# Kernel optimization log

Measured on AMD Instinct MI355X. Metric: run time of the kernel, lower is better.

## Reference

```python
import jax, jax.numpy as jnp
import numpy as np

N_NODES = 50000
N_EDGES = 1_600_000
D_IN, D_HID, D_OUT, K = 128, 50, 10, 5


def setup_inputs() -> dict:
    key = jax.random.key(0)
    ks = jax.random.split(key, 6)
    x = jax.random.normal(ks[0], (N_NODES, D_IN), dtype=jnp.float32)
    edge_index = jax.random.randint(ks[1], (2, N_EDGES), 0, N_NODES, dtype=jnp.int64)
    cheb_w = jax.random.normal(ks[2], (K, D_IN, D_HID), dtype=jnp.float32) * 0.05
    cheb_b = jax.random.normal(ks[3], (D_HID,), dtype=jnp.float32) * 0.05
    fc_w = jax.random.normal(ks[4], (D_HID, D_OUT), dtype=jnp.float32) * 0.1
    fc_b = jax.random.normal(ks[5], (D_OUT,), dtype=jnp.float32) * 0.1
    return {"x": x, "edge_index": edge_index, "cheb_w": cheb_w,
            "cheb_b": cheb_b, "fc_w": fc_w, "fc_b": fc_b}


def reference(x, edge_index, cheb_w, cheb_b, fc_w, fc_b):
    # ChebConv (PyG, normalization='sym', lambda_max=2.0):
    # L_hat = 2L/lambda_max - I = -D^{-1/2} A D^{-1/2} (zero diagonal)
    row, col = edge_index[0], edge_index[1]
    n = x.shape[0]
    deg = jax.ops.segment_sum(jnp.ones_like(row, dtype=x.dtype), row, num_segments=n)
    dinv = jnp.where(deg > 0, jax.lax.rsqrt(jnp.maximum(deg, 1.0)), 0.0)
    w = -dinv[row] * dinv[col]  # [E] edge weights of L_hat

    def prop(h):  # L_hat @ h via gather-scale-scatter
        return jax.ops.segment_sum(w[:, None] * h[col], row, num_segments=n)

    tx0 = x
    tx1 = prop(x)
    out = jnp.einsum('ni,io->no', tx0, cheb_w[0]) + jnp.einsum('ni,io->no', tx1, cheb_w[1])
    for k in range(2, K):
        tx2 = 2.0 * prop(tx1) - tx0
        out = out + jnp.einsum('ni,io->no', tx2, cheb_w[k])
        tx0, tx1 = tx1, tx2
    out = out + cheb_b

    h = jax.nn.relu(out)
    logits = h @ fc_w + fc_b
    return jax.nn.log_softmax(logits, axis=1)
```

## Files before the change

kernel.cpp:

```cpp
#include <hip/hip_runtime.h>
#include <hip/hip_fp16.h>

#define N_NODES 50000
#define N_EDGES 1600000
#define D_IN    128
#define D_HID   50
#define D_OUT   10
#define K_CHEB  5

#define P1_BLOCKS 256
#define EPB       (N_EDGES / P1_BLOCKS)
#define NBUCK2    256
#define NB_USED2  196
#define BCAP2     96

#define WH_ELEMS  (K_CHEB * 64 * D_IN)
#define WH_BLOCKS ((WH_ELEMS + 255) / 256)

#define VROW      64
#define VSTRIDE   ((size_t)(N_NODES + 1) * VROW)

typedef _Float16 half8_t __attribute__((ext_vector_type(8)));
typedef float    f32x4_t __attribute__((ext_vector_type(4)));


__global__ __launch_bounds__(256) void pass1_kernel(const int* __restrict__ row,
                                                    const int* __restrict__ col,
                                                    unsigned int* __restrict__ store,
                                                    int* __restrict__ bcnt,
                                                    const float* __restrict__ W,
                                                    __half* __restrict__ Wh,
                                                    __half* __restrict__ v,
                                                    __half* __restrict__ b1) {
    int tid = threadIdx.x;
    int blk = blockIdx.x;
    if (blk >= P1_BLOCKS) {
        int wb = blk - P1_BLOCKS;
        if (wb < WH_BLOCKS) {
            int idx = wb * 256 + tid;
            if (idx < WH_ELEMS) {
                int i = idx & 127;
                int n = (idx >> 7) & 63;
                int t = idx >> 13;
                float vv = (n < D_HID) ? W[t * D_IN * D_HID + i * D_HID + n] : 0.f;
                Wh[idx] = __float2half(vv);
            }
        } else {
            if (tid < VROW) {
                v[4 * VSTRIDE + (size_t)N_NODES * VROW + tid] = __float2half(0.f);
                b1[(size_t)N_NODES * VROW + tid] = __float2half(0.f);
            }
        }
        return;
    }
    __shared__ int cnt[NBUCK2];
    cnt[tid] = 0;
    __syncthreads();
    int base = blk * EPB;
    size_t sb = (size_t)blk * (NBUCK2 * BCAP2);
    for (int i = tid; i < EPB; i += 256) {
        int r = row[base + i];
        int c = col[base + i];
        int b = r >> 8;
        int pos = atomicAdd(&cnt[b], 1);
        if (pos >= BCAP2) pos = BCAP2 - 1;
        store[sb + b * BCAP2 + pos] = ((unsigned int)(r & 255) << 16) | (unsigned int)c;
    }
    __syncthreads();
    bcnt[blk * NBUCK2 + tid] = cnt[tid];
}

__global__ __launch_bounds__(512) void pass2_kernel(const unsigned int* __restrict__ store,
                                                    const int* __restrict__ bcnt,
                                                    int* __restrict__ row_start,
                                                    float* __restrict__ dinv,
                                                    float* __restrict__ dinv2,
                                                    float* __restrict__ sdeg,
                                                    int* __restrict__ ewc) {
    __shared__ int hist[256];
    __shared__ int off[256];
    __shared__ int fill[256];
    __shared__ int sb_part[512];
    __shared__ int pscan[256];
    __shared__ int s_bbase;
    int tid = threadIdx.x;
    int b = blockIdx.x;

    {
        int bt = tid & 255, seg = tid >> 8;
        int sum = 0;
        for (int s = seg * 128; s < seg * 128 + 128; ++s) sum += bcnt[s * NBUCK2 + bt];
        sb_part[tid] = sum;
    }
    __syncthreads();
    if (tid < 256) pscan[tid] = sb_part[tid] + sb_part[256 + tid];
    __syncthreads();
    for (int o = 1; o < 256; o <<= 1) {
        int vv = (tid < 256 && tid >= o) ? pscan[tid - o] : 0;
        __syncthreads();
        if (tid < 256) pscan[tid] += vv;
        __syncthreads();
    }
    if (tid == 0) {
        s_bbase = (b == 0) ? 0 : pscan[b - 1];
        if (b == 0) row_start[N_NODES] = pscan[255];
    }
    if (tid < 256) hist[tid] = 0;
    __syncthreads();
    int bbase_b = s_bbase;

    int strip = tid >> 1;
    int sub   = tid & 1;
    int sn = bcnt[strip * NBUCK2 + b];
    size_t sb = (size_t)strip * (NBUCK2 * BCAP2) + b * BCAP2;
    for (int i = sub; i < sn; i += 2)
        atomicAdd(&hist[store[sb + i] >> 16], 1);
    __syncthreads();
    int d = (tid < 256) ? hist[tid] : 0;
    if (tid < 256) off[tid] = d;
    __syncthreads();
    for (int o = 1; o < 256; o <<= 1) {
        int vv = (tid < 256 && tid >= o) ? off[tid - o] : 0;
        __syncthreads();
        if (tid < 256) off[tid] += vv;
        __syncthreads();
    }
    if (tid < 256) {
        int excl = off[tid] - d + bbase_b;
        hist[tid] = excl;
        fill[tid] = 0;
        int r = (b << 8) + tid;
        if (r < N_NODES) {
            row_start[r] = excl;
            float fd = (float)d;
            dinv[r]  = d ? rsqrtf(fd)  : 0.f;
            dinv2[r] = d ? (1.f / fd)  : 0.f;
            sdeg[r]  = d ? sqrtf(fd)   : 0.f;
        }
    }
    __syncthreads();
    for (int i = sub; i < sn; i += 2) {
        unsigned int vv = store[sb + i];
        int rl = vv >> 16;
        int c = vv & 0xffff;
        int p = atomicAdd(&fill[rl], 1);
        ewc[hist[rl] + p] = c;
    }
}

__global__ __launch_bounds__(256) void vgemm_kernel(const float* __restrict__ x,
                                                    const float* __restrict__ dinv,
                                                    const __half* __restrict__ Wh,
                                                    __half* __restrict__ v) {
    int tid = threadIdx.x;
    int lane = tid & 63;
    int wv = __builtin_amdgcn_readfirstlane(tid >> 6);
    int w = blockIdx.x * 4 + wv;
    int grp = w / 5;
    int t = w - grp * 5;
    int m = lane & 15;
    int quad = lane >> 4;

    int node = grp * 16 + m;
    bool ok = (node < N_NODES);
    int ln = ok ? node : (N_NODES - 1);
    float dv = ok ? dinv[node] : 0.f;

    half8_t bfr[4];
    #pragma unroll
    for (int ks = 0; ks < 4; ++ks) {
        const float4* xr = (const float4*)(x + (size_t)ln * D_IN + ks * 32 + quad * 8);
        float4 fA = xr[0], fB = xr[1];
        half8_t h;
        h[0] = (_Float16)fA.x; h[1] = (_Float16)fA.y;
        h[2] = (_Float16)fA.z; h[3] = (_Float16)fA.w;
        h[4] = (_Float16)fB.x; h[5] = (_Float16)fB.y;
        h[6] = (_Float16)fB.z; h[7] = (_Float16)fB.w;
        bfr[ks] = h;
    }

    const __half* Wt = Wh + t * (64 * D_IN);
    half8_t afr[4][4];
    #pragma unroll
    for (int ks = 0; ks < 4; ++ks) {
        int ko = ks * 32 + quad * 8;
        #pragma unroll
        for (int jt = 0; jt < 4; ++jt)
            afr[ks][jt] = *(const half8_t*)(Wt + (jt * 16 + m) * D_IN + ko);
    }

    f32x4_t acc[4];
    #pragma unroll
    for (int jt = 0; jt < 4; ++jt) acc[jt] = (f32x4_t)0.f;
    #pragma unroll
    for (int ks = 0; ks < 4; ++ks)
        #pragma unroll
        for (int jt = 0; jt < 4; ++jt)
            acc[jt] = __builtin_amdgcn_mfma_f32_16x16x32_f16(afr[ks][jt], bfr[ks], acc[jt], 0, 0, 0);

    if (ok) {
        __half* dst = v + t * VSTRIDE + (size_t)node * VROW + quad * 4;
        #pragma unroll
        for (int jt = 0; jt < 4; ++jt) {
            __half2 h0 = __float22half2_rn(make_float2(acc[jt][0] * dv, acc[jt][1] * dv));
            __half2 h1 = __float22half2_rn(make_float2(acc[jt][2] * dv, acc[jt][3] * dv));
            uint2 u;
            u.x = *(unsigned int*)&h0;
            u.y = *(unsigned int*)&h1;
            *(uint2*)(dst + jt * 16) = u;
        }
    }
}

__global__ __launch_bounds__(512) void prop_kernel(const int* __restrict__ row_start,
                                                   const int* __restrict__ ewc,
                                                   const float* __restrict__ dinv2,
                                                   const __half* __restrict__ src,
                                                   const __half* __restrict__ addv,
                                                   const __half* __restrict__ subv,
                                                   float alphaM, int do_sub,
                                                   __half* __restrict__ dst) {
    int tid = threadIdx.x;
    int lane = tid & 63;
    int wv = __builtin_amdgcn_readfirstlane(tid >> 6);
    int r = blockIdx.x * 8 + wv;
    int e0 = row_start[r], e1 = row_start[r + 1];
    float fac = -alphaM * dinv2[r];
    int l = lane & 7;
    int g = lane >> 3;
    const uint4* src16 = (const uint4*)src;
    float ac[8];
    #pragma unroll
    for (int j = 0; j < 8; ++j) ac[j] = 0.f;
    for (int e = e0; e < e1; e += 32) {
        #pragma unroll
        for (int i = 0; i < 4; ++i) {
            int base = e + 8 * i;
            int c0 = ewc[base + 0];
            int c1 = ewc[base + 1];
            int c2 = ewc[base + 2];
            int c3 = ewc[base + 3];
            int c4 = ewc[base + 4];
            int c5 = ewc[base + 5];
            int c6 = ewc[base + 6];
            int c7 = ewc[base + 7];
            int cA = (g & 1) ? c1 : c0;
            int cB = (g & 1) ? c3 : c2;
            int cC = (g & 1) ? c5 : c4;
            int cD = (g & 1) ? c7 : c6;
            int cE = (g & 2) ? cB : cA;
            int cF = (g & 2) ? cD : cC;
            int cl = (g & 4) ? cF : cE;
            if (base + g >= e1) cl = N_NODES;
            uint4 u = src16[(size_t)cl * 8 + l];
            float2 f0 = __half22float2(*(__half2*)&u.x);
            float2 f1 = __half22float2(*(__half2*)&u.y);
            float2 f2 = __half22float2(*(__half2*)&u.z);
            float2 f3 = __half22float2(*(__half2*)&u.w);
            ac[0] += f0.x; ac[1] += f0.y; ac[2] += f1.x; ac[3] += f1.y;
            ac[4] += f2.x; ac[5] += f2.y; ac[6] += f3.x; ac[7] += f3.y;
        }
    }
    #pragma unroll
    for (int k = 8; k <= 32; k <<= 1) {
        #pragma unroll
        for (int j = 0; j < 8; ++j) ac[j] += __shfl_xor(ac[j], k);
    }
    if (g == 0) {
        size_t o = (size_t)r * 8 + l;
        uint4 av = ((const uint4*)addv)[o];
        float2 av0 = __half22float2(*(__half2*)&av.x);
        float2 av1 = __half22float2(*(__half2*)&av.y);
        float2 av2 = __half22float2(*(__half2*)&av.z);
        float2 av3 = __half22float2(*(__half2*)&av.w);
        float r0 = av0.x + fac * ac[0];
        float r1 = av0.y + fac * ac[1];
        float r2 = av1.x + fac * ac[2];
        float r3 = av1.y + fac * ac[3];
        float r4 = av2.x + fac * ac[4];
        float r5 = av2.y + fac * ac[5];
        float r6 = av3.x + fac * ac[6];
        float r7 = av3.y + fac * ac[7];
        if (do_sub) {
            uint4 sv = ((const uint4*)subv)[o];
            float2 sv0 = __half22float2(*(__half2*)&sv.x);
            float2 sv1 = __half22float2(*(__half2*)&sv.y);
            float2 sv2 = __half22float2(*(__half2*)&sv.z);
            float2 sv3 = __half22float2(*(__half2*)&sv.w);
            r0 -= sv0.x; r1 -= sv0.y; r2 -= sv1.x; r3 -= sv1.y;
            r4 -= sv2.x; r5 -= sv2.y; r6 -= sv3.x; r7 -= sv3.y;
        }
        __half2 h0 = __float22half2_rn(make_float2(r0, r1));
        __half2 h1 = __float22half2_rn(make_float2(r2, r3));
        __half2 h2 = __float22half2_rn(make_float2(r4, r5));
        __half2 h3 = __float22half2_rn(make_float2(r6, r7));
        uint4 u;
        u.x = *(unsigned int*)&h0;
        u.y = *(unsigned int*)&h1;
        u.z = *(unsigned int*)&h2;
        u.w = *(unsigned int*)&h3;
        ((uint4*)dst)[o] = u;
    }
}

__global__ __launch_bounds__(256) void final_kernel(const __half* __restrict__ S,
                                                    const float* __restrict__ sdeg,
                                                    const float* __restrict__ cheb_b,
                                                    const float* __restrict__ fc_w,
                                                    const float* __restrict__ fc_b,
                                                    float* __restrict__ out) {
    int r = blockIdx.x * blockDim.x + threadIdx.x;
    if (r >= N_NODES) return;
    float sc = sdeg[r];
    const __half2* s2 = (const __half2*)(S + (size_t)r * VROW);
    float h[D_HID];
    #pragma unroll
    for (int i = 0; i < D_HID / 2; ++i) {
        float2 f = __half22float2(s2[i]);
        float v0 = sc * f.x + cheb_b[2 * i];
        float v1 = sc * f.y + cheb_b[2 * i + 1];
        h[2 * i]     = v0 > 0.f ? v0 : 0.f;
        h[2 * i + 1] = v1 > 0.f ? v1 : 0.f;
    }
    float lg[D_OUT];
    #pragma unroll
    for (int o = 0; o < D_OUT; ++o) lg[o] = fc_b[o];
    #pragma unroll 2
    for (int i = 0; i < D_HID; ++i) {
        float hv = h[i];
        #pragma unroll
        for (int o = 0; o < D_OUT; ++o) lg[o] += hv * fc_w[i * D_OUT + o];
    }
    float mx = lg[0];
    #pragma unroll
    for (int o = 1; o < D_OUT; ++o) mx = fmaxf(mx, lg[o]);
    float s = 0.f;
    #pragma unroll
    for (int o = 0; o < D_OUT; ++o) s += __expf(lg[o] - mx);
    float ls = __logf(s);
    size_t oo = (size_t)r * D_OUT;
    #pragma unroll
    for (int o = 0; o < D_OUT; ++o) out[oo + o] = lg[o] - mx - ls;
}

extern "C" void kernel_launch(void* const* d_in, const int* in_sizes, int n_in,
                              void* d_out, int out_size, void* d_ws, size_t ws_size,
                              hipStream_t stream) {
    const float* x      = (const float*)d_in[0];
    const int*   edge   = (const int*)d_in[1];
    const float* cheb_w = (const float*)d_in[2];
    const float* cheb_b = (const float*)d_in[3];
    const float* fc_w   = (const float*)d_in[4];
    const float* fc_b   = (const float*)d_in[5];
    float* out = (float*)d_out;

    const int* erow = edge;
    const int* ecol = edge + N_EDGES;

    uintptr_t p = ((uintptr_t)d_ws + 255) & ~(uintptr_t)255;
    auto alloc = [&](size_t bytes) {
        uintptr_t q = p;
        p = (p + bytes + 255) & ~(uintptr_t)255;
        return (void*)q;
    };
    unsigned int* store = (unsigned int*)alloc((size_t)P1_BLOCKS * NBUCK2 * BCAP2 * 4);
    int*    bcnt      = (int*)alloc((size_t)P1_BLOCKS * NBUCK2 * 4);
    int*    row_start = (int*)alloc((size_t)(N_NODES + 1) * 4);
    float*  dinv      = (float*)alloc((size_t)N_NODES * 4);
    float*  dinv2     = (float*)alloc((size_t)N_NODES * 4);
    float*  sdeg      = (float*)alloc((size_t)N_NODES * 4);
    int*    ewc       = (int*)alloc((size_t)(N_EDGES + 32) * 4);
    __half* Wh        = (__half*)alloc((size_t)WH_ELEMS * 2);
    __half* Sbuf      = (__half*)alloc(VSTRIDE * 2);
    __half* v         = (__half*)alloc(5 * VSTRIDE * 2);
    __half* b1        = (__half*)alloc(VSTRIDE * 2);

    __half* b3 = (__half*)store;
    __half* b2 = (__half*)store + VSTRIDE;
    __half* S  = Sbuf;

    pass1_kernel<<<P1_BLOCKS + WH_BLOCKS + 1, 256, 0, stream>>>(
        erow, ecol, store, bcnt, cheb_w, Wh, v, b1);
    pass2_kernel<<<NB_USED2, 512, 0, stream>>>(store, bcnt, row_start,
                                               dinv, dinv2, sdeg, ewc);
    hipMemsetAsync(b3 + (size_t)N_NODES * VROW, 0, VROW * 2, stream);
    hipMemsetAsync(b2 + (size_t)N_NODES * VROW, 0, VROW * 2, stream);

    const int NWAVE = ((N_NODES + 15) / 16) * K_CHEB;
    const int GBK = (NWAVE + 3) / 4;
    vgemm_kernel<<<GBK, 256, 0, stream>>>(x, dinv, Wh, v);

    __half* v0 = v;
    __half* v1 = v + 1 * VSTRIDE;
    __half* v2 = v + 2 * VSTRIDE;
    __half* v3 = v + 3 * VSTRIDE;
    __half* v4 = v + 4 * VSTRIDE;
    const int PB = N_NODES / 8;
    prop_kernel<<<PB, 512, 0, stream>>>(row_start, ewc, dinv2, v4, v3, v3, 2.f, 0, b3);
    prop_kernel<<<PB, 512, 0, stream>>>(row_start, ewc, dinv2, b3, v2, v4, 2.f, 1, b2);
    prop_kernel<<<PB, 512, 0, stream>>>(row_start, ewc, dinv2, b2, v1, b3, 2.f, 1, b1);
    prop_kernel<<<PB, 512, 0, stream>>>(row_start, ewc, dinv2, b1, v0, b2, 1.f, 1, S);

    final_kernel<<<(N_NODES + 255) / 256, 256, 0, stream>>>(S, sdeg, cheb_b,
                                                            fc_w, fc_b, out);
}
```

Before: 311.6 us.

## Make vgemm persistent per weight slice with prefetched x rows; per-lane edge index load

The vgemm kernel now launches a fixed set of waves for each Chebyshev weight slice. Each wave loads its weight fragments once and walks node groups with a stride, prefetching the next group's x rows while running MFMAs on the current one. This amortises the weight fragment loads and hides x load latency, but it removes the bounds check, relying on N_NODES being divisible by 16. In prop_kernel, the eight scalar index loads and select tree are replaced by one per-lane indexed load of the edge column.

```diff
diff --git a/kernel.cpp b/kernel.cpp
--- a/kernel.cpp
+++ b/kernel.cpp
@@ -19,6 +19,10 @@
 
 #define VROW      64
 #define VSTRIDE   ((size_t)(N_NODES + 1) * VROW)
+
+#define NGROUP    (N_NODES / 16)
+#define VG_SPAN   512
+#define VG_WAVES  (K_CHEB * VG_SPAN)
 
 typedef _Float16 half8_t __attribute__((ext_vector_type(8)));
 typedef float    f32x4_t __attribute__((ext_vector_type(4)));
@@ -156,29 +160,11 @@
     int lane = tid & 63;
     int wv = __builtin_amdgcn_readfirstlane(tid >> 6);
     int w = blockIdx.x * 4 + wv;
-    int grp = w / 5;
-    int t = w - grp * 5;
+    int t = w / VG_SPAN;
+    int idx = w - t * VG_SPAN;
     int m = lane & 15;
     int quad = lane >> 4;
 
-    int node = grp * 16 + m;
-    bool ok = (node < N_NODES);
-    int ln = ok ? node : (N_NODES - 1);
-    float dv = ok ? dinv[node] : 0.f;
-
-    half8_t bfr[4];
-    #pragma unroll
-    for (int ks = 0; ks < 4; ++ks) {
-        const float4* xr = (const float4*)(x + (size_t)ln * D_IN + ks * 32 + quad * 8);
-        float4 fA = xr[0], fB = xr[1];
-        half8_t h;
-        h[0] = (_Float16)fA.x; h[1] = (_Float16)fA.y;
-        h[2] = (_Float16)fA.z; h[3] = (_Float16)fA.w;
-        h[4] = (_Float16)fB.x; h[5] = (_Float16)fB.y;
-        h[6] = (_Float16)fB.z; h[7] = (_Float16)fB.w;
-        bfr[ks] = h;
-    }
-
     const __half* Wt = Wh + t * (64 * D_IN);
     half8_t afr[4][4];
     #pragma unroll
@@ -189,17 +175,51 @@
             afr[ks][jt] = *(const half8_t*)(Wt + (jt * 16 + m) * D_IN + ko);
     }
 
-    f32x4_t acc[4];
-    #pragma unroll
-    for (int jt = 0; jt < 4; ++jt) acc[jt] = (f32x4_t)0.f;
-    #pragma unroll
-    for (int ks = 0; ks < 4; ++ks)
-        #pragma unroll
-        for (int jt = 0; jt < 4; ++jt)
-            acc[jt] = __builtin_amdgcn_mfma_f32_16x16x32_f16(afr[ks][jt], bfr[ks], acc[jt], 0, 0, 0);
-
-    if (ok) {
-        __half* dst = v + t * VSTRIDE + (size_t)node * VROW + quad * 4;
+    __half* vt = v + t * VSTRIDE;
+
+    float4 pf[8];
+    int g = idx;
+    {
+        const float* xr = x + (size_t)(g * 16 + m) * D_IN;
+        #pragma unroll
+        for (int ks = 0; ks < 4; ++ks) {
+            pf[2 * ks]     = *(const float4*)(xr + ks * 32 + quad * 8);
+            pf[2 * ks + 1] = *(const float4*)(xr + ks * 32 + quad * 8 + 4);
+        }
+    }
+
+    for (; g < NGROUP; g += VG_SPAN) {
+        int node = g * 16 + m;
+        float dv = dinv[node];
+        half8_t bfr[4];
+        #pragma unroll
+        for (int ks = 0; ks < 4; ++ks) {
+            float4 fA = pf[2 * ks], fB = pf[2 * ks + 1];
+            half8_t h;
+            h[0] = (_Float16)fA.x; h[1] = (_Float16)fA.y;
+            h[2] = (_Float16)fA.z; h[3] = (_Float16)fA.w;
+            h[4] = (_Float16)fB.x; h[5] = (_Float16)fB.y;
+            h[6] = (_Float16)fB.z; h[7] = (_Float16)fB.w;
+            bfr[ks] = h;
+        }
+        int gn = g + VG_SPAN;
+        if (gn < NGROUP) {
+            const float* xr = x + (size_t)(gn * 16 + m) * D_IN;
+            #pragma unroll
+            for (int ks = 0; ks < 4; ++ks) {
+                pf[2 * ks]     = *(const float4*)(xr + ks * 32 + quad * 8);
+                pf[2 * ks + 1] = *(const float4*)(xr + ks * 32 + quad * 8 + 4);
+            }
+        }
+        f32x4_t acc[4];
+        #pragma unroll
+        for (int jt = 0; jt < 4; ++jt) acc[jt] = (f32x4_t)0.f;
+        #pragma unroll
+        for (int ks = 0; ks < 4; ++ks)
+            #pragma unroll
+            for (int jt = 0; jt < 4; ++jt)
+                acc[jt] = __builtin_amdgcn_mfma_f32_16x16x32_f16(afr[ks][jt], bfr[ks], acc[jt], 0, 0, 0);
+        __half* dst = vt + (size_t)node * VROW + quad * 4;
         #pragma unroll
         for (int jt = 0; jt < 4; ++jt) {
             __half2 h0 = __float22half2_rn(make_float2(acc[jt][0] * dv, acc[jt][1] * dv));
@@ -236,21 +256,7 @@
         #pragma unroll
         for (int i = 0; i < 4; ++i) {
             int base = e + 8 * i;
-            int c0 = ewc[base + 0];
-            int c1 = ewc[base + 1];
-            int c2 = ewc[base + 2];
-            int c3 = ewc[base + 3];
-            int c4 = ewc[base + 4];
-            int c5 = ewc[base + 5];
-            int c6 = ewc[base + 6];
-            int c7 = ewc[base + 7];
-            int cA = (g & 1) ? c1 : c0;
-            int cB = (g & 1) ? c3 : c2;
-            int cC = (g & 1) ? c5 : c4;
-            int cD = (g & 1) ? c7 : c6;
-            int cE = (g & 2) ? cB : cA;
-            int cF = (g & 2) ? cD : cC;
-            int cl = (g & 4) ? cF : cE;
+            int cl = ewc[base + g];
             if (base + g >= e1) cl = N_NODES;
             uint4 u = src16[(size_t)cl * 8 + l];
             float2 f0 = __half22float2(*(__half2*)&u.x);
@@ -386,9 +392,7 @@
     hipMemsetAsync(b3 + (size_t)N_NODES * VROW, 0, VROW * 2, stream);
     hipMemsetAsync(b2 + (size_t)N_NODES * VROW, 0, VROW * 2, stream);
 
-    const int NWAVE = ((N_NODES + 15) / 16) * K_CHEB;
-    const int GBK = (NWAVE + 3) / 4;
-    vgemm_kernel<<<GBK, 256, 0, stream>>>(x, dinv, Wh, v);
+    vgemm_kernel<<<VG_WAVES / 4, 256, 0, stream>>>(x, dinv, Wh, v);
 
     __half* v0 = v;
     __half* v1 = v + 1 * VSTRIDE;
```

Result: faster. 291.9 us (-6.3%).
